# Performance work log

Hardware: AMD Instinct MI355X
Metric: run time of the kernel (lower is better)

The kernel has to match this reference:

```python
import jax, jax.numpy as jnp
import numpy as np

B, T, C = 4, 2048, 1024
N_HEAD = 16


def setup_inputs() -> dict:
    key = jax.random.key(0)
    k1, k2, k3, k4, k5 = jax.random.split(key, 5)
    x = jax.random.normal(k1, (B, T, C), dtype=jnp.float32)
    # c_attn: Dense(3*C) -> kernel [C, 3C], bias [3C]
    w_attn = jax.random.normal(k2, (C, 3 * C), dtype=jnp.float32) * 0.02
    b_attn = jnp.zeros((3 * C,), dtype=jnp.float32)
    # c_proj: Dense(C) with scaled init 0.02/sqrt(2*n_layer), n_layer=24
    w_proj = jax.random.normal(k3, (C, C), dtype=jnp.float32) * (0.02 / np.sqrt(2 * 24))
    b_proj = jnp.zeros((C,), dtype=jnp.float32)
    return {"x": x, "w_attn": w_attn, "b_attn": b_attn, "w_proj": w_proj, "b_proj": b_proj}


def reference(x, w_attn, b_attn, w_proj, b_proj):
    Bx, Tx, Cx = x.shape
    hd = Cx // N_HEAD  # head dim
    qkv = x @ w_attn + b_attn                      # [B, T, 3C]
    q, k, v = jnp.split(qkv, 3, axis=2)
    q = q.reshape(Bx, Tx, N_HEAD, hd).transpose(0, 2, 1, 3)  # [B, H, T, hd]
    k = k.reshape(Bx, Tx, N_HEAD, hd).transpose(0, 2, 1, 3)
    v = v.reshape(Bx, Tx, N_HEAD, hd).transpose(0, 2, 1, 3)
    mask = jnp.tril(jnp.ones((1, 1, Tx, Tx), dtype=bool))
    att = jnp.einsum('bhqd,bhkd->bhqk', q, k) / jnp.sqrt(jnp.float32(hd))
    att = jnp.where(mask, att, jnp.finfo(jnp.float32).min)
    att = jax.nn.softmax(att, axis=-1)
    y = jnp.einsum('bhqk,bhkd->bhqd', att, v)      # [B, H, T, hd]
    y = y.transpose(0, 2, 1, 3).reshape(Bx, Tx, Cx)
    return y @ w_proj + b_proj
```

## Files before the change

kernel.cpp:

```cpp
#include <hip/hip_runtime.h>
#include <cstdint>
#include <cstddef>

typedef unsigned short u16;
typedef __bf16 bf16_t;
typedef bf16_t bf16x8 __attribute__((ext_vector_type(8)));
typedef float f32x4 __attribute__((ext_vector_type(4)));

__device__ __forceinline__ u16 f32_to_bf16(float f) {
  uint32_t u = __builtin_bit_cast(uint32_t, f);
  u += 0x7fffu + ((u >> 16) & 1u);
  return (u16)(u >> 16);
}

__device__ __forceinline__ uint32_t pack_bf16x2(float lo, float hi) {
  uint32_t a = __builtin_bit_cast(uint32_t, hi) + 0x8000u;
  uint32_t b = __builtin_bit_cast(uint32_t, lo) + 0x8000u;
  return __builtin_amdgcn_perm(a, b, 0x07060302u);
}

__device__ __forceinline__ void gload_lds16(const void* g, void* l) {
  __builtin_amdgcn_global_load_lds(
      (const __attribute__((address_space(1))) unsigned int*)g,
      (__attribute__((address_space(3))) unsigned int*)l, 16, 0, 0);
}

__global__ void cvt_bf16(const float* __restrict__ in, u16* __restrict__ out, int n) {
  int i = (blockIdx.x * 256 + threadIdx.x) * 4;
  if (i < n) {
    float4 f = *(const float4*)(in + i);
    ushort4 o;
    o.x = f32_to_bf16(f.x); o.y = f32_to_bf16(f.y);
    o.z = f32_to_bf16(f.z); o.w = f32_to_bf16(f.w);
    *(ushort4*)(out + i) = o;
  }
}

__global__ void tconv(const float* __restrict__ in, u16* __restrict__ out, int R, int C) {
  __shared__ u16 t[64][80];
  int tid = threadIdx.x;
  int cb = blockIdx.x * 64, rb = blockIdx.y * 64;
  int rr = tid >> 2, cg = (tid & 3) * 16;
  const float* ip = in + (size_t)(rb + rr) * C + cb + cg;
#pragma unroll
  for (int i = 0; i < 16; ++i) t[rr][cg + i] = f32_to_bf16(ip[i]);
  __syncthreads();
  int cc = tid >> 2, rg = (tid & 3) * 16;
  u16* op = out + (size_t)(cb + cc) * R + rb + rg;
  union { uint4 v[2]; u16 s[16]; } tmp;
#pragma unroll
  for (int i = 0; i < 16; ++i) tmp.s[i] = t[rg + i][cc];
  *(uint4*)op = tmp.v[0];
  *(uint4*)(op + 8) = tmp.v[1];
}

__global__ void vtrans(const u16* __restrict__ qkvb, u16* __restrict__ vt) {
  __shared__ u16 t[64][80];
  int tid = threadIdx.x;
  int bh = blockIdx.x, tb = blockIdx.y * 64;
  int b = bh >> 4, h = bh & 15;
  int tt = tid >> 2, dg = (tid & 3) * 16;
  const u16* ip = qkvb + (size_t)(b * 2048 + tb + tt) * 3072 + 2048 + h * 64 + dg;
  union { uint4 v; u16 s[8]; } a0, a1;
  a0.v = *(const uint4*)ip;
  a1.v = *(const uint4*)(ip + 8);
#pragma unroll
  for (int i = 0; i < 8; ++i) { t[tt][dg + i] = a0.s[i]; t[tt][dg + 8 + i] = a1.s[i]; }
  __syncthreads();
  int dd = tid >> 2, tg = (tid & 3) * 16;
  u16* op = vt + (size_t)(bh * 64 + dd) * 2048 + tb + tg;
  union { uint4 v[2]; u16 s[16]; } tmp;
#pragma unroll
  for (int i = 0; i < 16; ++i) tmp.s[i] = t[tg + i][dd];
  *(uint4*)op = tmp.v[0];
  *(uint4*)(op + 8) = tmp.v[1];
}

template <int OUT_BF16>
__global__ __launch_bounds__(512, 2) void gemm256(const u16* __restrict__ A,
                                                  const u16* __restrict__ Bt,
                                                  const float* __restrict__ bias,
                                                  void* __restrict__ Cout,
                                                  int M, int N, int K) {
  __shared__ __align__(16) u16 lds[2][2][16384];
  const int tid = threadIdx.x;
  const int w = tid >> 6, L = tid & 63;
  const int quad = L >> 4, lc = L & 15;
  const int wr = w >> 2, wc = w & 3;
  const int wrM = wr * 128, wcN = wc * 64;
  const int rL = L >> 3;
  const int gsw = (L & 7) ^ rL;

  const int nbx = N >> 8;
  const int cpx = gridDim.x >> 3;
  const int id = blockIdx.x;
  const int swz = (id & 7) * cpx + (id >> 3);
  const int tileN = (swz % nbx) << 8;
  const int tileM = (swz / nbx) << 8;
  const int nkt = K >> 6;

  u16* const A0 = &lds[0][0][0];
  u16* const B0 = &lds[0][1][0];
  u16* const A1 = &lds[1][0][0];
  u16* const B1 = &lds[1][1][0];

  auto stageQ = [&](const u16* Mp, int gRow, int kt, u16* reg) {
    int ktc = kt < nkt ? kt : nkt - 1;
    const u16* src = Mp + (size_t)(gRow + w * 8 + rL) * K + (ktc << 6) + gsw * 8;
    gload_lds16(src, reg + w * 512);
  };

  f32x4 acc[8][4] = {};
  const int rsw = lc & 7;
  const int g0 = (quad ^ rsw) * 8;
  const int g1 = ((4 + quad) ^ rsw) * 8;
  const int aRow = (wrM + lc) * 64;
  const int bRow = (wcN + lc) * 64;

  stageQ(A, tileM + 0, 0, A0 + 0);
  stageQ(A, tileM + 128, 0, A0 + 8192);
  stageQ(Bt, tileN + 0, 0, B0 + 0);
  stageQ(Bt, tileN + 64, 0, B0 + 4096);
  stageQ(A, tileM + 64, 0, A0 + 4096);
  stageQ(A, tileM + 192, 0, A0 + 12288);
  stageQ(Bt, tileN + 128, 0, B0 + 8192);
  stageQ(Bt, tileN + 192, 0, B0 + 12288);
  stageQ(A, tileM + 0, 1, A1 + 0);
  stageQ(A, tileM + 128, 1, A1 + 8192);
  stageQ(Bt, tileN + 0, 1, B1 + 0);
  stageQ(Bt, tileN + 64, 1, B1 + 4096);
  stageQ(A, tileM + 64, 1, A1 + 4096);
  stageQ(A, tileM + 192, 1, A1 + 12288);
  asm volatile("s_waitcnt vmcnt(6)" ::: "memory");
  __builtin_amdgcn_s_barrier();

  auto group = [&](u16* Ab, u16* Bb, u16* Bob, int T) {
    bf16x8 af[4][2], blo[2][2], bhi[2][2];
#pragma unroll
    for (int mi = 0; mi < 4; ++mi) {
      af[mi][0] = *(const bf16x8*)&Ab[aRow + mi * 1024 + g0];
      af[mi][1] = *(const bf16x8*)&Ab[aRow + mi * 1024 + g1];
    }
#pragma unroll
    for (int ni = 0; ni < 2; ++ni) {
      blo[ni][0] = *(const bf16x8*)&Bb[bRow + ni * 1024 + g0];
      blo[ni][1] = *(const bf16x8*)&Bb[bRow + ni * 1024 + g1];
    }
    stageQ(Bt, tileN + 128, T + 1, Bob + 8192);
    stageQ(Bt, tileN + 192, T + 1, Bob + 12288);
    asm volatile("" ::: "memory");
    __builtin_amdgcn_s_barrier();
    asm volatile("s_waitcnt lgkmcnt(0)" ::: "memory");
    __builtin_amdgcn_s_setprio(1);
#pragma unroll
    for (int mi = 0; mi < 4; ++mi)
#pragma unroll
      for (int ni = 0; ni < 2; ++ni) {
        acc[mi][ni] = __builtin_amdgcn_mfma_f32_16x16x32_bf16(af[mi][0], blo[ni][0], acc[mi][ni], 0, 0, 0);
        acc[mi][ni] = __builtin_amdgcn_mfma_f32_16x16x32_bf16(af[mi][1], blo[ni][1], acc[mi][ni], 0, 0, 0);
      }
    __builtin_amdgcn_s_setprio(0);
    asm volatile("" ::: "memory");
    __builtin_amdgcn_s_barrier();
#pragma unroll
    for (int ni = 0; ni < 2; ++ni) {
      bhi[ni][0] = *(const bf16x8*)&Bb[bRow + (2 + ni) * 1024 + g0];
      bhi[ni][1] = *(const bf16x8*)&Bb[bRow + (2 + ni) * 1024 + g1];
    }
    stageQ(A, tileM + 0, T + 2, Ab + 0);
    stageQ(A, tileM + 128, T + 2, Ab + 8192);
    asm volatile("" ::: "memory");
    __builtin_amdgcn_s_barrier();
    asm volatile("s_waitcnt lgkmcnt(0)" ::: "memory");
    __builtin_amdgcn_s_setprio(1);
#pragma unroll
    for (int mi = 0; mi < 4; ++mi)
#pragma unroll
      for (int ni = 0; ni < 2; ++ni) {
        acc[mi][ni + 2] = __builtin_amdgcn_mfma_f32_16x16x32_bf16(af[mi][0], bhi[ni][0], acc[mi][ni + 2], 0, 0, 0);
        acc[mi][ni + 2] = __builtin_amdgcn_mfma_f32_16x16x32_bf16(af[mi][1], bhi[ni][1], acc[mi][ni + 2], 0, 0, 0);
      }
    __builtin_amdgcn_s_setprio(0);
    asm volatile("" ::: "memory");
    __builtin_amdgcn_s_barrier();
#pragma unroll
    for (int mi = 0; mi < 4; ++mi) {
      af[mi][0] = *(const bf16x8*)&Ab[aRow + (4 + mi) * 1024 + g0];
      af[mi][1] = *(const bf16x8*)&Ab[aRow + (4 + mi) * 1024 + g1];
    }
    stageQ(Bt, tileN + 0, T + 2, Bb + 0);
    stageQ(Bt, tileN + 64, T + 2, Bb + 4096);
    asm volatile("" ::: "memory");
    __builtin_amdgcn_s_barrier();
    asm volatile("s_waitcnt lgkmcnt(0)" ::: "memory");
    __builtin_amdgcn_s_setprio(1);
#pragma unroll
    for (int mi = 0; mi < 4; ++mi)
#pragma unroll
      for (int ni = 0; ni < 2; ++ni) {
        acc[mi + 4][ni + 2] = __builtin_amdgcn_mfma_f32_16x16x32_bf16(af[mi][0], bhi[ni][0], acc[mi + 4][ni + 2], 0, 0, 0);
        acc[mi + 4][ni + 2] = __builtin_amdgcn_mfma_f32_16x16x32_bf16(af[mi][1], bhi[ni][1], acc[mi + 4][ni + 2], 0, 0, 0);
      }
    __builtin_amdgcn_s_setprio(0);
    asm volatile("" ::: "memory");
    __builtin_amdgcn_s_barrier();
    stageQ(A, tileM + 64, T + 2, Ab + 4096);
    stageQ(A, tileM + 192, T + 2, Ab + 12288);
    asm volatile("" ::: "memory");
    __builtin_amdgcn_s_barrier();
    __builtin_amdgcn_s_setprio(1);
#pragma unroll
    for (int mi = 0; mi < 4; ++mi)
#pragma unroll
      for (int ni = 0; ni < 2; ++ni) {
        acc[mi + 4][ni] = __builtin_amdgcn_mfma_f32_16x16x32_bf16(af[mi][0], blo[ni][0], acc[mi + 4][ni], 0, 0, 0);
        acc[mi + 4][ni] = __builtin_amdgcn_mfma_f32_16x16x32_bf16(af[mi][1], blo[ni][1], acc[mi + 4][ni], 0, 0, 0);
      }
    __builtin_amdgcn_s_setprio(0);
    asm volatile("s_waitcnt vmcnt(6)" ::: "memory");
    __builtin_amdgcn_s_barrier();
  };

  for (int T = 0; T < nkt; T += 2) {
    group(A0, B0, B1, T);
    group(A1, B1, B0, T + 1);
  }

  asm volatile("s_waitcnt vmcnt(0)" ::: "memory");

#pragma unroll
  for (int mi = 0; mi < 8; ++mi) {
    int rowb = tileM + wrM + mi * 16 + quad * 4;
#pragma unroll
    for (int ni = 0; ni < 4; ++ni) {
      int col = tileN + wcN + ni * 16 + lc;
      float bv = bias[col];
#pragma unroll
      for (int r = 0; r < 4; ++r) {
        float v = acc[mi][ni][r] + bv;
        if (OUT_BF16)
          ((u16*)Cout)[(size_t)(rowb + r) * N + col] = f32_to_bf16(v);
        else
          ((float*)Cout)[(size_t)(rowb + r) * N + col] = v;
      }
    }
  }
}

__global__ __launch_bounds__(256, 4) void attn(const u16* __restrict__ qkvb,
                                               const u16* __restrict__ vt,
                                               u16* __restrict__ yb) {
  __shared__ __align__(16) u16 kv[2][16][512];
  __shared__ __align__(16) u16 pbuf[4][1024];
  const int tid = threadIdx.x;
  const int w = tid >> 6, L = tid & 63;
  const int quad = L >> 4, lc = L & 15;
  const int bh = blockIdx.x;
  const int b = bh >> 4, h = bh & 15;
  const int pair = blockIdx.y;
  const float e_c = 0.18033688f;
  u16* pb = (u16*)pbuf[w];

  const bool isK = (w < 2);
  const u16* sbase = isK
      ? qkvb + ((size_t)(b * 2048 + w * 32 + lc) * 3072 + 1024 + h * 64 + quad * 8)
      : vt + ((size_t)(bh * 64 + (w - 2) * 32 + lc) * 2048 + quad * 8);
  const size_t fo1 = isK ? (size_t)16 * 3072 : (size_t)16 * 2048;

  auto stage = [&](int nkb, int buf) {
    const u16* s = sbase + (isK ? (size_t)nkb * 3072 : (size_t)nkb);
    u16* d = &kv[buf][w * 4][0];
    gload_lds16(s, d);
    gload_lds16(s + 32, d + 512);
    gload_lds16(s + fo1, d + 1024);
    gload_lds16(s + fo1 + 32, d + 1536);
  };

  int par = 0;
  stage(0, 0);

  for (int pass = 0; pass < 2; ++pass) {
    const int qt = pass ? (31 - pair) : pair;
    const int qbase = qt * 64;
    const int q_loc = w * 16 + lc;

    bf16x8 qf[2];
    {
      const u16* qp = qkvb + ((size_t)(b * 2048 + qbase + q_loc) * 3072 + h * 64 + quad * 8);
      qf[0] = *(const bf16x8*)qp;
      qf[1] = *(const bf16x8*)(qp + 32);
    }
    f32x4 o[4] = {};
    float lsum = 0.f;

    for (int kb = 0; kb <= qbase; kb += 64) {
      const bool diag = (kb == qbase);
      __syncthreads();
      const int nkb = (kb < qbase) ? kb + 64 : 0;
      stage(nkb, par ^ 1);

      f32x4 s[4];
      __builtin_amdgcn_s_setprio(1);
#pragma unroll
      for (int nt = 0; nt < 4; ++nt) {
        s[nt] = (f32x4){0.f, 0.f, 0.f, 0.f};
#pragma unroll
        for (int ks = 0; ks < 2; ++ks) {
          bf16x8 kf = *(const bf16x8*)&kv[par][nt * 2 + ks][L * 8];
          s[nt] = __builtin_amdgcn_mfma_f32_16x16x32_bf16(kf, qf[ks], s[nt], 0, 0, 0);
        }
      }
      __builtin_amdgcn_s_setprio(0);

#pragma unroll
      for (int nt = 0; nt < 4; ++nt) {
        float p0 = __builtin_amdgcn_exp2f(s[nt][0] * e_c);
        float p1 = __builtin_amdgcn_exp2f(s[nt][1] * e_c);
        float p2 = __builtin_amdgcn_exp2f(s[nt][2] * e_c);
        float p3 = __builtin_amdgcn_exp2f(s[nt][3] * e_c);
        if (diag) {
          int tk0 = nt * 16 + quad * 4;
          p0 = (tk0 + 0 > q_loc) ? 0.f : p0;
          p1 = (tk0 + 1 > q_loc) ? 0.f : p1;
          p2 = (tk0 + 2 > q_loc) ? 0.f : p2;
          p3 = (tk0 + 3 > q_loc) ? 0.f : p3;
        }
        lsum += (p0 + p1) + (p2 + p3);
        uint2 pk;
        pk.x = pack_bf16x2(p0, p1);
        pk.y = pack_bf16x2(p2, p3);
        int idx = (nt >> 1) * 512 + (((nt & 1) * 2 + (quad >> 1)) * 16 + lc) * 8 + (quad & 1) * 4;
        *(uint2*)&pb[idx] = pk;
      }

      __builtin_amdgcn_s_setprio(1);
#pragma unroll
      for (int ks = 0; ks < 2; ++ks) {
        bf16x8 pf = *(const bf16x8*)&pb[ks * 512 + L * 8];
#pragma unroll
        for (int dt = 0; dt < 4; ++dt) {
          bf16x8 vf = *(const bf16x8*)&kv[par][8 + dt * 2 + ks][L * 8];
          o[dt] = __builtin_amdgcn_mfma_f32_16x16x32_bf16(vf, pf, o[dt], 0, 0, 0);
        }
      }
      __builtin_amdgcn_s_setprio(0);

      par ^= 1;
    }

    lsum += __shfl_xor(lsum, 16);
    lsum += __shfl_xor(lsum, 32);
    float inv = 1.f / lsum;

    {
      u16* yp = yb + (size_t)(b * 2048 + qbase + q_loc) * 1024 + h * 64 + quad * 4;
#pragma unroll
      for (int dt = 0; dt < 4; ++dt) {
        uint2 pk;
        pk.x = pack_bf16x2(o[dt][0] * inv, o[dt][1] * inv);
        pk.y = pack_bf16x2(o[dt][2] * inv, o[dt][3] * inv);
        *(uint2*)(yp + dt * 16) = pk;
      }
    }
  }

  asm volatile("s_waitcnt vmcnt(0)" ::: "memory");
}

extern "C" void kernel_launch(void* const* d_in, const int* in_sizes, int n_in,
                              void* d_out, int out_size, void* d_ws, size_t ws_size,
                              hipStream_t stream) {
  const float* x = (const float*)d_in[0];
  const float* w_attn = (const float*)d_in[1];
  const float* b_attn = (const float*)d_in[2];
  const float* w_proj = (const float*)d_in[3];
  const float* b_proj = (const float*)d_in[4];
  float* out = (float*)d_out;

  char* ws = (char*)d_ws;
  u16* xb = (u16*)ws;    ws += (size_t)8192 * 1024 * 2;
  u16* waT = (u16*)ws;   ws += (size_t)3072 * 1024 * 2;
  u16* wpT = (u16*)ws;   ws += (size_t)1024 * 1024 * 2;
  u16* qkvb = (u16*)ws;  ws += (size_t)8192 * 3072 * 2;
  u16* vtb = (u16*)ws;   ws += (size_t)64 * 64 * 2048 * 2;
  u16* yb = (u16*)ws;    ws += (size_t)8192 * 1024 * 2;

  cvt_bf16<<<8192, 256, 0, stream>>>(x, xb, 8192 * 1024);
  tconv<<<dim3(3072 / 64, 1024 / 64), 256, 0, stream>>>(w_attn, waT, 1024, 3072);
  tconv<<<dim3(1024 / 64, 1024 / 64), 256, 0, stream>>>(w_proj, wpT, 1024, 1024);
  gemm256<1><<<dim3(384), 512, 0, stream>>>(xb, waT, b_attn, qkvb, 8192, 3072, 1024);
  vtrans<<<dim3(64, 32), 256, 0, stream>>>(qkvb, vtb);
  attn<<<dim3(64, 16), 256, 0, stream>>>(qkvb, vtb, yb);
  gemm256<0><<<dim3(128), 512, 0, stream>>>(yb, wpT, b_proj, out, 8192, 1024, 1024);
}
```

Measured before the change: 272.4 us.

## Switch attention to 32x32x16 MFMA with register-resident P and 2-wave blocks

Rewrites the attention kernel to use 32x32x16 bf16 MFMA tiles with two waves per block, each wave owning 32 query rows. The softmax probabilities stay in registers and feed the PV MFMA directly, which removes the per-wave LDS P buffer and its round trip. The V transpose kernel permutes its element order to match the new operand layout. In exchange, each block has half as many waves and each wave holds more registers, which may lower occupancy and latency hiding.

```diff
diff --git a/kernel.cpp b/kernel.cpp
--- a/kernel.cpp
+++ b/kernel.cpp
@@ -6,6 +6,7 @@
 typedef __bf16 bf16_t;
 typedef bf16_t bf16x8 __attribute__((ext_vector_type(8)));
 typedef float f32x4 __attribute__((ext_vector_type(4)));
+typedef float f32x16 __attribute__((ext_vector_type(16)));
 
 __device__ __forceinline__ u16 f32_to_bf16(float f) {
   uint32_t u = __builtin_bit_cast(uint32_t, f);
@@ -71,7 +72,10 @@
   u16* op = vt + (size_t)(bh * 64 + dd) * 2048 + tb + tg;
   union { uint4 v[2]; u16 s[16]; } tmp;
 #pragma unroll
-  for (int i = 0; i < 16; ++i) tmp.s[i] = t[tg + i][dd];
+  for (int i = 0; i < 16; ++i) {
+    int pi = (i & 3) | ((i & 4) << 1) | ((i & 8) >> 1);
+    tmp.s[i] = t[tg + pi][dd];
+  }
   *(uint4*)op = tmp.v[0];
   *(uint4*)(op + 8) = tmp.v[1];
 }
@@ -247,33 +251,34 @@
   }
 }
 
-__global__ __launch_bounds__(256, 4) void attn(const u16* __restrict__ qkvb,
+__global__ __launch_bounds__(128, 2) void attn(const u16* __restrict__ qkvb,
                                                const u16* __restrict__ vt,
                                                u16* __restrict__ yb) {
   __shared__ __align__(16) u16 kv[2][16][512];
-  __shared__ __align__(16) u16 pbuf[4][1024];
   const int tid = threadIdx.x;
   const int w = tid >> 6, L = tid & 63;
-  const int quad = L >> 4, lc = L & 15;
+  const int l5 = L & 31, hi = L >> 5;
   const int bh = blockIdx.x;
   const int b = bh >> 4, h = bh & 15;
   const int pair = blockIdx.y;
   const float e_c = 0.18033688f;
-  u16* pb = (u16*)pbuf[w];
-
-  const bool isK = (w < 2);
-  const u16* sbase = isK
-      ? qkvb + ((size_t)(b * 2048 + w * 32 + lc) * 3072 + 1024 + h * 64 + quad * 8)
-      : vt + ((size_t)(bh * 64 + (w - 2) * 32 + lc) * 2048 + quad * 8);
-  const size_t fo1 = isK ? (size_t)16 * 3072 : (size_t)16 * 2048;
-
-  auto stage = [&](int nkb, int buf) {
-    const u16* s = sbase + (isK ? (size_t)nkb * 3072 : (size_t)nkb);
-    u16* d = &kv[buf][w * 4][0];
-    gload_lds16(s, d);
-    gload_lds16(s + 32, d + 512);
-    gload_lds16(s + fo1, d + 1024);
-    gload_lds16(s + fo1 + 32, d + 1536);
+
+  const bool isK = (w == 0);
+  const u16* kbase = qkvb + ((size_t)(b * 2048 + l5) * 3072 + 1024 + h * 64 + hi * 8);
+  const u16* vbase = vt + ((size_t)(bh * 64 + l5) * 2048 + hi * 8);
+
+  auto stage = [&](int kb2, int buf) {
+    if (isK) {
+#pragma unroll
+      for (int i = 0; i < 8; ++i)
+        gload_lds16(kbase + (size_t)(kb2 + (i >> 2) * 32) * 3072 + (i & 3) * 16,
+                    &kv[buf][i][0]);
+    } else {
+#pragma unroll
+      for (int i = 0; i < 8; ++i)
+        gload_lds16(vbase + (size_t)((i >> 2) * 32) * 2048 + kb2 + (i & 3) * 16,
+                    &kv[buf][8 + i][0]);
+    }
   };
 
   int par = 0;
@@ -282,85 +287,85 @@
   for (int pass = 0; pass < 2; ++pass) {
     const int qt = pass ? (31 - pair) : pair;
     const int qbase = qt * 64;
-    const int q_loc = w * 16 + lc;
-
-    bf16x8 qf[2];
+    const int qrow = qbase + w * 32 + l5;
+    const int lim = w * 32 + l5 - hi * 4;
+
+    bf16x8 qf[4];
     {
-      const u16* qp = qkvb + ((size_t)(b * 2048 + qbase + q_loc) * 3072 + h * 64 + quad * 8);
-      qf[0] = *(const bf16x8*)qp;
-      qf[1] = *(const bf16x8*)(qp + 32);
-    }
-    f32x4 o[4] = {};
+      const u16* qp = qkvb + ((size_t)(b * 2048 + qrow) * 3072 + h * 64 + hi * 8);
+#pragma unroll
+      for (int ds = 0; ds < 4; ++ds) qf[ds] = *(const bf16x8*)(qp + ds * 16);
+    }
+    f32x16 o0 = {}, o1 = {};
     float lsum = 0.f;
 
     for (int kb = 0; kb <= qbase; kb += 64) {
       const bool diag = (kb == qbase);
       __syncthreads();
-      const int nkb = (kb < qbase) ? kb + 64 : 0;
-      stage(nkb, par ^ 1);
-
-      f32x4 s[4];
+      stage((kb < qbase) ? kb + 64 : 0, par ^ 1);
+
+      f32x16 st0 = {}, st1 = {};
       __builtin_amdgcn_s_setprio(1);
 #pragma unroll
-      for (int nt = 0; nt < 4; ++nt) {
-        s[nt] = (f32x4){0.f, 0.f, 0.f, 0.f};
-#pragma unroll
-        for (int ks = 0; ks < 2; ++ks) {
-          bf16x8 kf = *(const bf16x8*)&kv[par][nt * 2 + ks][L * 8];
-          s[nt] = __builtin_amdgcn_mfma_f32_16x16x32_bf16(kf, qf[ks], s[nt], 0, 0, 0);
+      for (int ds = 0; ds < 4; ++ds) {
+        bf16x8 k0 = *(const bf16x8*)&kv[par][ds][L * 8];
+        bf16x8 k1 = *(const bf16x8*)&kv[par][4 + ds][L * 8];
+        st0 = __builtin_amdgcn_mfma_f32_32x32x16_bf16(k0, qf[ds], st0, 0, 0, 0);
+        st1 = __builtin_amdgcn_mfma_f32_32x32x16_bf16(k1, qf[ds], st1, 0, 0, 0);
+      }
+      __builtin_amdgcn_s_setprio(0);
+
+#pragma unroll
+      for (int r = 0; r < 16; ++r) {
+        float p0 = __builtin_amdgcn_exp2f(st0[r] * e_c);
+        float p1 = __builtin_amdgcn_exp2f(st1[r] * e_c);
+        if (diag) {
+          const int br = (r & 3) + 8 * (r >> 2);
+          p0 = (br <= lim) ? p0 : 0.f;
+          p1 = (32 + br <= lim) ? p1 : 0.f;
         }
+        st0[r] = p0;
+        st1[r] = p1;
+        lsum += p0 + p1;
+      }
+
+      __builtin_amdgcn_s_setprio(1);
+#pragma unroll
+      for (int sg = 0; sg < 2; ++sg) {
+        union { uint32_t u[4]; bf16x8 v; } pf0, pf1;
+#pragma unroll
+        for (int q2 = 0; q2 < 4; ++q2) {
+          pf0.u[q2] = pack_bf16x2(st0[sg * 8 + q2 * 2], st0[sg * 8 + q2 * 2 + 1]);
+          pf1.u[q2] = pack_bf16x2(st1[sg * 8 + q2 * 2], st1[sg * 8 + q2 * 2 + 1]);
+        }
+        const int ks0 = sg, ks1 = 2 + sg;
+        bf16x8 va = *(const bf16x8*)&kv[par][8 + ks0][L * 8];
+        bf16x8 vb = *(const bf16x8*)&kv[par][12 + ks0][L * 8];
+        o0 = __builtin_amdgcn_mfma_f32_32x32x16_bf16(va, pf0.v, o0, 0, 0, 0);
+        o1 = __builtin_amdgcn_mfma_f32_32x32x16_bf16(vb, pf0.v, o1, 0, 0, 0);
+        va = *(const bf16x8*)&kv[par][8 + ks1][L * 8];
+        vb = *(const bf16x8*)&kv[par][12 + ks1][L * 8];
+        o0 = __builtin_amdgcn_mfma_f32_32x32x16_bf16(va, pf1.v, o0, 0, 0, 0);
+        o1 = __builtin_amdgcn_mfma_f32_32x32x16_bf16(vb, pf1.v, o1, 0, 0, 0);
       }
       __builtin_amdgcn_s_setprio(0);
 
-#pragma unroll
-      for (int nt = 0; nt < 4; ++nt) {
-        float p0 = __builtin_amdgcn_exp2f(s[nt][0] * e_c);
-        float p1 = __builtin_amdgcn_exp2f(s[nt][1] * e_c);
-        float p2 = __builtin_amdgcn_exp2f(s[nt][2] * e_c);
-        float p3 = __builtin_amdgcn_exp2f(s[nt][3] * e_c);
-        if (diag) {
-          int tk0 = nt * 16 + quad * 4;
-          p0 = (tk0 + 0 > q_loc) ? 0.f : p0;
-          p1 = (tk0 + 1 > q_loc) ? 0.f : p1;
-          p2 = (tk0 + 2 > q_loc) ? 0.f : p2;
-          p3 = (tk0 + 3 > q_loc) ? 0.f : p3;
-        }
-        lsum += (p0 + p1) + (p2 + p3);
-        uint2 pk;
-        pk.x = pack_bf16x2(p0, p1);
-        pk.y = pack_bf16x2(p2, p3);
-        int idx = (nt >> 1) * 512 + (((nt & 1) * 2 + (quad >> 1)) * 16 + lc) * 8 + (quad & 1) * 4;
-        *(uint2*)&pb[idx] = pk;
-      }
-
-      __builtin_amdgcn_s_setprio(1);
-#pragma unroll
-      for (int ks = 0; ks < 2; ++ks) {
-        bf16x8 pf = *(const bf16x8*)&pb[ks * 512 + L * 8];
-#pragma unroll
-        for (int dt = 0; dt < 4; ++dt) {
-          bf16x8 vf = *(const bf16x8*)&kv[par][8 + dt * 2 + ks][L * 8];
-          o[dt] = __builtin_amdgcn_mfma_f32_16x16x32_bf16(vf, pf, o[dt], 0, 0, 0);
-        }
-      }
-      __builtin_amdgcn_s_setprio(0);
-
       par ^= 1;
     }
 
-    lsum += __shfl_xor(lsum, 16);
     lsum += __shfl_xor(lsum, 32);
     float inv = 1.f / lsum;
 
-    {
-      u16* yp = yb + (size_t)(b * 2048 + qbase + q_loc) * 1024 + h * 64 + quad * 4;
-#pragma unroll
-      for (int dt = 0; dt < 4; ++dt) {
-        uint2 pk;
-        pk.x = pack_bf16x2(o[dt][0] * inv, o[dt][1] * inv);
-        pk.y = pack_bf16x2(o[dt][2] * inv, o[dt][3] * inv);
-        *(uint2*)(yp + dt * 16) = pk;
-      }
+    u16* yp = yb + (size_t)(b * 2048 + qrow) * 1024 + h * 64 + hi * 4;
+#pragma unroll
+    for (int g = 0; g < 4; ++g) {
+      uint2 pk;
+      pk.x = pack_bf16x2(o0[g * 4 + 0] * inv, o0[g * 4 + 1] * inv);
+      pk.y = pack_bf16x2(o0[g * 4 + 2] * inv, o0[g * 4 + 3] * inv);
+      *(uint2*)(yp + g * 8) = pk;
+      pk.x = pack_bf16x2(o1[g * 4 + 0] * inv, o1[g * 4 + 1] * inv);
+      pk.y = pack_bf16x2(o1[g * 4 + 2] * inv, o1[g * 4 + 3] * inv);
+      *(uint2*)(yp + 32 + g * 8) = pk;
     }
   }
 
@@ -390,6 +395,6 @@
   tconv<<<dim3(1024 / 64, 1024 / 64), 256, 0, stream>>>(w_proj, wpT, 1024, 1024);
   gemm256<1><<<dim3(384), 512, 0, stream>>>(xb, waT, b_attn, qkvb, 8192, 3072, 1024);
   vtrans<<<dim3(64, 32), 256, 0, stream>>>(qkvb, vtb);
-  attn<<<dim3(64, 16), 256, 0, stream>>>(qkvb, vtb, yb);
+  attn<<<dim3(64, 16), 128, 0, stream>>>(qkvb, vtb, yb);
   gemm256<0><<<dim3(128), 512, 0, stream>>>(yb, wpT, b_proj, out, 8192, 1024, 1024);
 }
```

Measured after the change: 273.7 us. About the same (+0.5%).
